# Kernel optimization log

Hardware: AMD Instinct MI355X
Metric: run time of the kernel (lower is better)

Reference implementation:

```python
import jax, jax.numpy as jnp
import numpy as np
from jax import lax

NUM_CLASSES = 5
NUM_TASKS = 20
CONV_CHANS = [(64, 3), (64, 64), (128, 64), (128, 128), (256, 128), (256, 256)]  # (out, in)


def setup_inputs() -> dict:
    key = jax.random.key(0)
    ks = jax.random.split(key, 16)
    B = 512
    x = jax.random.normal(ks[0], (B, 3, 32, 32), dtype=jnp.float32)
    tid = jax.random.randint(ks[1], (B,), 0, NUM_TASKS)
    inp = {"x": x, "tid": tid}
    for i, (oc, ic) in enumerate(CONV_CHANS):
        fan_in = ic * 9
        inp[f"w{i}"] = jax.random.normal(ks[2 + 2 * i], (oc, ic, 3, 3), dtype=jnp.float32) * np.float32((2.0 / fan_in) ** 0.5)
        inp[f"b{i}"] = jnp.zeros((oc,), dtype=jnp.float32)
    inp["cw"] = jax.random.normal(ks[14], (NUM_CLASSES * NUM_TASKS, 4096), dtype=jnp.float32) * np.float32(4096 ** -0.5)
    inp["cb"] = jnp.zeros((NUM_CLASSES * NUM_TASKS,), dtype=jnp.float32)
    return inp


def _conv_relu(x, w, b):
    y = lax.conv_general_dilated(x, w, window_strides=(1, 1), padding='SAME',
                                 dimension_numbers=('NCHW', 'OIHW', 'NCHW'))
    return jax.nn.relu(y + b[None, :, None, None])


def _maxpool2(x):
    return lax.reduce_window(x, -jnp.inf, lax.max, (1, 1, 2, 2), (1, 1, 2, 2), 'VALID')


def _forward(x, tid, ws, bs, cw, cb):
    # VGG cfg [64,64,'M',128,128,'M',256,256,'M']
    h = _conv_relu(x, ws[0], bs[0])
    h = _conv_relu(h, ws[1], bs[1])
    h = _maxpool2(h)
    h = _conv_relu(h, ws[2], bs[2])
    h = _conv_relu(h, ws[3], bs[3])
    h = _maxpool2(h)
    h = _conv_relu(h, ws[4], bs[4])
    h = _conv_relu(h, ws[5], bs[5])
    h = _maxpool2(h)                      # [B, 256, 4, 4]
    feat = h.reshape(h.shape[0], -1)      # [B, 4096], matches torch NCHW flatten
    # Batched task-indexed classifier: gather each sample's 5-row weight block.
    w_sel = cw.reshape(NUM_TASKS, NUM_CLASSES, 4096)[tid]   # [B, 5, 4096]
    b_sel = cb.reshape(NUM_TASKS, NUM_CLASSES)[tid]         # [B, 5]
    return jnp.einsum('bcd,bd->bc', w_sel, feat) + b_sel


def reference(x, tid, w0, b0, w1, b1, w2, b2, w3, b3, w4, b4, w5, b5, cw, cb):
    ws = (w0, w1, w2, w3, w4, w5)
    bs = (b0, b1, b2, b3, b4, b5)
    return _forward(x, tid, ws, bs, cw, cb)
```

## Files before the change

### kernel.cpp

```cpp
#include <hip/hip_runtime.h>


typedef __attribute__((ext_vector_type(8))) short short8;
typedef __attribute__((ext_vector_type(4))) float floatx4;
typedef unsigned int uint;
typedef unsigned short ushort;

__device__ __forceinline__ ushort f2bf(float f) {
    uint u = __float_as_uint(f);
    return (ushort)((u + 0x7fffu + ((u >> 16) & 1u)) >> 16);
}
__device__ __forceinline__ float bf2f(ushort h) {
    return __uint_as_float(((uint)h) << 16);
}

__global__ __launch_bounds__(256) void wtransform_lin(
    const float* __restrict__ src, short* __restrict__ dst, int OC, int IC)
{
    int n = 9 * OC * IC;
    int o = blockIdx.x * 256 + threadIdx.x;
    if (o >= n) return;
    int j    = o & 7;
    int lane = (o >> 3) & 63;
    int r    = o >> 9;
    int G16  = OC >> 4;
    int g    = r % G16;  r /= G16;
    int kk   = r % 9;
    int icb  = r / 9;
    int oc = g * 16 + (lane & 15);
    int ic = icb * 32 + (lane >> 4) * 8 + j;
    dst[o] = (short)f2bf(src[((long)oc * IC + ic) * 9 + kk]);
}

__global__ __launch_bounds__(256) void wtransform0(
    const float* __restrict__ src, short* __restrict__ dst)
{
    int idx = blockIdx.x * 256 + threadIdx.x;
    if (idx >= 64 * 32) return;
    int oc = idx >> 5, k = idx & 31;
    dst[idx] = (k < 27) ? (short)f2bf(src[oc * 27 + k]) : (short)0;
}

__global__ __launch_bounds__(256, 2) void conv0_mfma(
    const float* __restrict__ x, const short* __restrict__ wT0,
    const float* __restrict__ b0, ushort* __restrict__ out)
{
    __shared__ float  s_x[3 * 18 * 34];
    __shared__ ushort s_b[4 * 512 * 8];

    const int tid  = threadIdx.x;
    const int wv   = tid >> 6;
    const int lane = tid & 63;
    const int quad = lane >> 4;
    const int l16  = lane & 15;
    const int b    = blockIdx.x >> 1;
    const int r0   = (blockIdx.x & 1) * 16;

    for (int idx = tid; idx < 3 * 18 * 34; idx += 256) {
        int c   = idx / 612;
        int rem = idx - c * 612;
        int ry  = rem / 34, rx = rem - ry * 34;
        int gy  = r0 + ry - 1, gx = rx - 1;
        float v = 0.f;
        if (gy >= 0 && gy < 32 && gx >= 0 && gx < 32)
            v = x[(((long)b * 3 + c) * 32 + gy) * 32 + gx];
        s_x[idx] = v;
    }
    __syncthreads();

#pragma unroll
    for (int rep = 0; rep < 2; ++rep) {
        int pxl = rep * 256 + tid;
        int py = pxl >> 5, px = pxl & 31;
        ushort v[32];
#pragma unroll
        for (int c = 0; c < 3; ++c)
#pragma unroll
            for (int ky = 0; ky < 3; ++ky)
#pragma unroll
                for (int kx = 0; kx < 3; ++kx)
                    v[c * 9 + ky * 3 + kx] = f2bf(s_x[c * 612 + (py + ky) * 34 + (px + kx)]);
#pragma unroll
        for (int k = 27; k < 32; ++k) v[k] = 0;
#pragma unroll
        for (int q = 0; q < 4; ++q)
            *(uint4*)(&s_b[(q * 512 + pxl) * 8]) = *(const uint4*)(v + q * 8);
    }
    __syncthreads();

    floatx4 acc[4][8];
#pragma unroll
    for (int i = 0; i < 4; ++i)
#pragma unroll
        for (int t = 0; t < 8; ++t) acc[i][t] = (floatx4)0.f;

    short8 afr[4];
#pragma unroll
    for (int i = 0; i < 4; ++i)
        afr[i] = *(const short8*)(wT0 + (i * 16 + l16) * 32 + quad * 8);
#pragma unroll
    for (int t = 0; t < 8; ++t) {
        int pxl = wv * 128 + t * 16 + l16;
        short8 bfr = *(const short8*)(&s_b[(quad * 512 + pxl) * 8]);
#pragma unroll
        for (int i = 0; i < 4; ++i)
            acc[i][t] = __builtin_amdgcn_mfma_f32_16x16x32_bf16(afr[i], bfr, acc[i][t], 0, 0, 0);
    }

#pragma unroll
    for (int i = 0; i < 4; ++i) {
        int oc0 = i * 16 + quad * 4;
        float4 bv = *(const float4*)(b0 + oc0);
#pragma unroll
        for (int t = 0; t < 8; ++t) {
            int pxl = wv * 128 + t * 16 + l16;
            int py = pxl >> 5, px = pxl & 31;
            long dst = ((((long)b * 8 + (oc0 >> 3)) * 32 + r0 + py) * 32 + px) * 8 + (oc0 & 7);
            float v0 = acc[i][t][0] + bv.x;
            float v1 = acc[i][t][1] + bv.y;
            float v2 = acc[i][t][2] + bv.z;
            float v3 = acc[i][t][3] + bv.w;
            ushort o[4];
            o[0] = f2bf(v0 > 0.f ? v0 : 0.f);
            o[1] = f2bf(v1 > 0.f ? v1 : 0.f);
            o[2] = f2bf(v2 > 0.f ? v2 : 0.f);
            o[3] = f2bf(v3 > 0.f ? v3 : 0.f);
            *(uint2*)(out + dst) = *(uint2*)o;
        }
    }
}

template<int IC, int OC, int H, int W, int ROWS, int OCGROUPS, bool POOL>
__global__ __launch_bounds__(256, 2) void conv_so(
    const ushort* __restrict__ act_in,
    const short*  __restrict__ wTs,
    const float*  __restrict__ bias,
    ushort* __restrict__ act_out)
{
    constexpr int WPAD  = W + 2;
    constexpr int RPAD  = ROWS + 2;
    constexpr int UNITS = RPAD * WPAD;
    constexpr int SEGS  = H / ROWS;
    constexpr int C8I   = IC / 8;
    constexpr int CPUP  = C8I + 1;
    constexpr int G16   = OC / 16;
    constexpr int NICB  = IC / 32;
    constexpr int C8O   = OC / 8;
    constexpr int TMAX  = NICB * 9;

    __shared__ ushort s_act[UNITS * CPUP * 8];

    const int tid  = threadIdx.x;
    const int wv   = tid >> 6;
    const int lane = tid & 63;
    const int quad = lane >> 4;
    const int l16  = lane & 15;

    const int b   = blockIdx.x / SEGS;
    const int seg = blockIdx.x - b * SEGS;
    const int r0  = seg * ROWS;
    const int ocg = wv % OCGROUPS;
    const int pxg = wv / OCGROUPS;

    for (int c = tid; c < UNITS * C8I; c += 256) {
        int sub  = c / UNITS;
        int unit = c - sub * UNITS;
        int ry   = unit / WPAD, cx = unit - ry * WPAD;
        int gy   = r0 + ry - 1, gx = cx - 1;
        uint4 val = make_uint4(0, 0, 0, 0);
        if ((unsigned)gy < (unsigned)H && (unsigned)gx < (unsigned)W) {
            long src = ((((long)b * C8I + sub) * H + gy) * W + gx) * 8;
            val = *(const uint4*)(act_in + src);
        }
        *(uint4*)(&s_act[((size_t)unit * CPUP + sub) * 8]) = val;
    }
    __syncthreads();

    floatx4 acc[4][4];
#pragma unroll
    for (int i = 0; i < 4; ++i)
#pragma unroll
        for (int t = 0; t < 4; ++t) acc[i][t] = (floatx4)0.f;

    int bbase[4];
#pragma unroll
    for (int t = 0; t < 4; ++t) {
        int pxl = pxg * 64 + t * 16 + l16;
        int py  = pxl / W, px = pxl - py * W;
        bbase[t] = (py * WPAD + px) * CPUP * 8;
    }

    const short8* wb = (const short8*)wTs;
    short8 afr[4];
#pragma unroll
    for (int i = 0; i < 4; ++i)
        afr[i] = wb[((long)0 * G16 + ocg * 4 + i) * 64 + lane];

    int tl = 0;
    for (int icb = 0; icb < NICB; ++icb) {
#pragma unroll
        for (int kk = 0; kk < 9; ++kk) {
            const int ky = kk / 3, kx = kk - ky * 3;
            const int koff = ((ky * WPAD + kx) * CPUP + icb * 4 + quad) * 8;
            short8 bfr[4];
#pragma unroll
            for (int t = 0; t < 4; ++t)
                bfr[t] = *(const short8*)(&s_act[bbase[t] + koff]);
            int tn = (tl + 1 < TMAX) ? tl + 1 : tl;
            short8 afrN[4];
#pragma unroll
            for (int i = 0; i < 4; ++i)
                afrN[i] = wb[((long)tn * G16 + ocg * 4 + i) * 64 + lane];
#pragma unroll
            for (int i = 0; i < 4; ++i)
#pragma unroll
                for (int t = 0; t < 4; ++t)
                    acc[i][t] = __builtin_amdgcn_mfma_f32_16x16x32_bf16(
                        afr[i], bfr[t], acc[i][t], 0, 0, 0);
#pragma unroll
            for (int i = 0; i < 4; ++i) afr[i] = afrN[i];
            ++tl;
        }
    }

    if constexpr (!POOL) {
#pragma unroll
        for (int i = 0; i < 4; ++i) {
            int oc0 = ocg * 64 + i * 16 + quad * 4;
            float4 bv = *(const float4*)(bias + oc0);
#pragma unroll
            for (int t = 0; t < 4; ++t) {
                int pxl = pxg * 64 + t * 16 + l16;
                int py  = pxl / W, px = pxl - py * W;
                long dst = ((((long)b * C8O + (oc0 >> 3)) * H + r0 + py) * W + px) * 8 + (oc0 & 7);
                float v0 = acc[i][t][0] + bv.x;
                float v1 = acc[i][t][1] + bv.y;
                float v2 = acc[i][t][2] + bv.z;
                float v3 = acc[i][t][3] + bv.w;
                ushort o[4];
                o[0] = f2bf(v0 > 0.f ? v0 : 0.f);
                o[1] = f2bf(v1 > 0.f ? v1 : 0.f);
                o[2] = f2bf(v2 > 0.f ? v2 : 0.f);
                o[3] = f2bf(v3 > 0.f ? v3 : 0.f);
                *(uint2*)(act_out + dst) = *(uint2*)o;
            }
        }
    } else {
        __syncthreads();
        ushort* s_pool = s_act;
        constexpr int PSTR = OC + 8;
        static_assert(ROWS * W * PSTR <= UNITS * CPUP * 8, "pool scratch fits");
#pragma unroll
        for (int i = 0; i < 4; ++i) {
            int oc0 = ocg * 64 + i * 16 + quad * 4;
            float4 bv = *(const float4*)(bias + oc0);
#pragma unroll
            for (int t = 0; t < 4; ++t) {
                int pxl = pxg * 64 + t * 16 + l16;
                float v0 = acc[i][t][0] + bv.x;
                float v1 = acc[i][t][1] + bv.y;
                float v2 = acc[i][t][2] + bv.z;
                float v3 = acc[i][t][3] + bv.w;
                ushort o[4];
                o[0] = f2bf(v0 > 0.f ? v0 : 0.f);
                o[1] = f2bf(v1 > 0.f ? v1 : 0.f);
                o[2] = f2bf(v2 > 0.f ? v2 : 0.f);
                o[3] = f2bf(v3 > 0.f ? v3 : 0.f);
                *(uint2*)(&s_pool[pxl * PSTR + oc0]) = *(uint2*)o;
            }
        }
        __syncthreads();
        constexpr int PH = ROWS / 2, PW = W / 2, HOT = H / 2;
        const int pr0 = r0 / 2;
        for (int u = tid; u < PH * PW * C8O; u += 256) {
            int c8 = u % C8O;
            int pp = u / C8O;
            int xo = pp % PW, yo = pp / PW;
            const ushort* p00 = &s_pool[((2 * yo) * W + 2 * xo) * PSTR + c8 * 8];
            uint4 q0 = *(const uint4*)(p00);
            uint4 q1 = *(const uint4*)(p00 + PSTR);
            uint4 q2 = *(const uint4*)(p00 + W * PSTR);
            uint4 q3 = *(const uint4*)(p00 + W * PSTR + PSTR);
            const ushort* a0 = (const ushort*)&q0;
            const ushort* a1 = (const ushort*)&q1;
            const ushort* a2 = (const ushort*)&q2;
            const ushort* a3 = (const ushort*)&q3;
            ushort r[8];
#pragma unroll
            for (int j = 0; j < 8; ++j) {
                ushort m0 = a0[j] > a1[j] ? a0[j] : a1[j];
                ushort m1 = a2[j] > a3[j] ? a2[j] : a3[j];
                r[j] = m0 > m1 ? m0 : m1;
            }
            long dst = ((((long)b * C8O + c8) * HOT + pr0 + yo) * PW + xo) * 8;
            *(uint4*)(act_out + dst) = *(uint4*)r;
        }
    }
}

__global__ __launch_bounds__(256) void classifier_k(
    const ushort* __restrict__ feat, const int* __restrict__ tids,
    const float* __restrict__ cw, const float* __restrict__ cb,
    float* __restrict__ out, int B)
{
    int g = blockIdx.x * 256 + threadIdx.x;
    int wid = g >> 6, lane = g & 63;
    if (wid >= B * 5) return;
    int b = wid / 5, c = wid - b * 5;
    int t = tids[b];
    const float* wrow = cw + (long)(t * 5 + c) * 4096;
    const ushort* f = feat + (long)b * 4096;
    float s = 0.f;
#pragma unroll 4
    for (int d = lane; d < 4096; d += 64) {
        int fidx = (((d >> 7) * 16) + (d & 15)) * 8 + ((d >> 4) & 7);
        s += wrow[d] * bf2f(f[fidx]);
    }
#pragma unroll
    for (int off = 32; off > 0; off >>= 1) s += __shfl_down(s, off, 64);
    if (lane == 0) out[wid] = s + cb[t * 5 + c];
}

extern "C" void kernel_launch(void* const* d_in, const int* in_sizes, int n_in,
                              void* d_out, int out_size, void* d_ws, size_t ws_size,
                              hipStream_t stream)
{
    const float* x   = (const float*)d_in[0];
    const int*   tid = (const int*)d_in[1];
    const float* w0 = (const float*)d_in[2];  const float* b0 = (const float*)d_in[3];
    const float* w1 = (const float*)d_in[4];  const float* b1 = (const float*)d_in[5];
    const float* w2 = (const float*)d_in[6];  const float* b2 = (const float*)d_in[7];
    const float* w3 = (const float*)d_in[8];  const float* b3 = (const float*)d_in[9];
    const float* w4 = (const float*)d_in[10]; const float* b4 = (const float*)d_in[11];
    const float* w5 = (const float*)d_in[12]; const float* b5 = (const float*)d_in[13];
    const float* cw = (const float*)d_in[14];
    const float* cb = (const float*)d_in[15];
    float* outp = (float*)d_out;

    const int B = in_sizes[0] / (3 * 32 * 32);

    short* wt0  = (short*)d_ws;
    short* wts1 = wt0 + 2048;
    short* wts2 = wts1 + 36864;
    short* wts3 = wts2 + 73728;
    short* wts4 = wts3 + 147456;
    short* wts5 = wts4 + 294912;
    const size_t WT_HW = 2048 + 36864 + 73728 + 147456 + 294912 + 589824;
    const size_t fixed_bytes = WT_HW * 2;

    int Bc = B;
    while (Bc > 2 && fixed_bytes + (size_t)Bc * 2 * 65536 * 2 > ws_size) Bc >>= 1;
    if (Bc < 2) Bc = 2;

    ushort* bufA = (ushort*)((short*)d_ws + WT_HW);
    ushort* bufB = bufA + (size_t)Bc * 65536;

    wtransform0<<<(64 * 32 + 255) / 256, 256, 0, stream>>>(w0, wt0);
    wtransform_lin<<<(9 * 64 * 64 + 255) / 256, 256, 0, stream>>>(w1, wts1, 64, 64);
    wtransform_lin<<<(9 * 128 * 64 + 255) / 256, 256, 0, stream>>>(w2, wts2, 128, 64);
    wtransform_lin<<<(9 * 128 * 128 + 255) / 256, 256, 0, stream>>>(w3, wts3, 128, 128);
    wtransform_lin<<<(9 * 256 * 128 + 255) / 256, 256, 0, stream>>>(w4, wts4, 256, 128);
    wtransform_lin<<<(9 * 256 * 256 + 255) / 256, 256, 0, stream>>>(w5, wts5, 256, 256);

    for (int cb0 = 0; cb0 < B; cb0 += Bc) {
        const float* xc = x + (size_t)cb0 * 3 * 32 * 32;
        const int* tidc = tid + cb0;
        float* outc = outp + (size_t)cb0 * 5;

        conv0_mfma<<<Bc * 2, 256, 0, stream>>>(xc, wt0, b0, bufA);
        conv_so<64, 64, 32, 32, 8, 1, true><<<Bc * 4, 256, 0, stream>>>(bufA, wts1, b1, bufB);
        conv_so<64, 128, 16, 16, 8, 2, false><<<Bc * 2, 256, 0, stream>>>(bufB, wts2, b2, bufA);
        conv_so<128, 128, 16, 16, 8, 2, true><<<Bc * 2, 256, 0, stream>>>(bufA, wts3, b3, bufB);
        conv_so<128, 256, 8, 8, 8, 4, false><<<Bc, 256, 0, stream>>>(bufB, wts4, b4, bufA);
        conv_so<256, 256, 8, 8, 8, 4, true><<<Bc, 256, 0, stream>>>(bufA, wts5, b5, bufB);
        classifier_k<<<(Bc * 5 * 64 + 255) / 256, 256, 0, stream>>>(bufB, tidc, cw, cb, outc, Bc);
    }
}
```

Baseline: 316.0 us.

## Deepen weight prefetch to three stages, raise occupancy, fuse weight transforms

The conv kernel now keeps a three-deep ring of weight fragments in registers, issuing each global load three kernel taps ahead instead of one, to hide global-load latency behind the MFMAs. Launch bounds are raised to three blocks per SM, which caps registers per thread even though the deeper prefetch needs more of them, so spilling is a risk. The six weight-transform launches are merged into one kernel to cut launch overhead. The ring index uses kk%3 inside the unrolled 9-tap loop, so it is compile-time and the ring stays in registers.

```diff
diff --git a/kernel.cpp b/kernel.cpp
--- a/kernel.cpp
+++ b/kernel.cpp
@@ -14,12 +14,9 @@
     return __uint_as_float(((uint)h) << 16);
 }
 
-__global__ __launch_bounds__(256) void wtransform_lin(
-    const float* __restrict__ src, short* __restrict__ dst, int OC, int IC)
-{
-    int n = 9 * OC * IC;
-    int o = blockIdx.x * 256 + threadIdx.x;
-    if (o >= n) return;
+__device__ __forceinline__ void wlin_one(
+    const float* __restrict__ src, short* __restrict__ dst, int OC, int IC, int o)
+{
     int j    = o & 7;
     int lane = (o >> 3) & 63;
     int r    = o >> 9;
@@ -32,13 +29,37 @@
     dst[o] = (short)f2bf(src[((long)oc * IC + ic) * 9 + kk]);
 }
 
-__global__ __launch_bounds__(256) void wtransform0(
-    const float* __restrict__ src, short* __restrict__ dst)
+#define N_W0 2048
+#define N_W1 36864
+#define N_W2 73728
+#define N_W3 147456
+#define N_W4 294912
+#define N_W5 589824
+#define N_WT_TOTAL (N_W0 + N_W1 + N_W2 + N_W3 + N_W4 + N_W5)
+
+__global__ __launch_bounds__(256) void wtransform_all(
+    const float* __restrict__ w0, const float* __restrict__ w1,
+    const float* __restrict__ w2, const float* __restrict__ w3,
+    const float* __restrict__ w4, const float* __restrict__ w5,
+    short* __restrict__ wt0, short* __restrict__ wts1, short* __restrict__ wts2,
+    short* __restrict__ wts3, short* __restrict__ wts4, short* __restrict__ wts5)
 {
     int idx = blockIdx.x * 256 + threadIdx.x;
-    if (idx >= 64 * 32) return;
-    int oc = idx >> 5, k = idx & 31;
-    dst[idx] = (k < 27) ? (short)f2bf(src[oc * 27 + k]) : (short)0;
+    if (idx < N_W0) {
+        int oc = idx >> 5, k = idx & 31;
+        wt0[idx] = (k < 27) ? (short)f2bf(w0[oc * 27 + k]) : (short)0;
+        return;
+    }
+    idx -= N_W0;
+    if (idx < N_W1) { wlin_one(w1, wts1, 64, 64, idx); return; }
+    idx -= N_W1;
+    if (idx < N_W2) { wlin_one(w2, wts2, 128, 64, idx); return; }
+    idx -= N_W2;
+    if (idx < N_W3) { wlin_one(w3, wts3, 128, 128, idx); return; }
+    idx -= N_W3;
+    if (idx < N_W4) { wlin_one(w4, wts4, 256, 128, idx); return; }
+    idx -= N_W4;
+    wlin_one(w5, wts5, 256, 256, idx);
 }
 
 __global__ __launch_bounds__(256, 2) void conv0_mfma(
@@ -131,7 +152,7 @@
 }
 
 template<int IC, int OC, int H, int W, int ROWS, int OCGROUPS, bool POOL>
-__global__ __launch_bounds__(256, 2) void conv_so(
+__global__ __launch_bounds__(256, 3) void conv_so(
     const ushort* __restrict__ act_in,
     const short*  __restrict__ wTs,
     const float*  __restrict__ bias,
@@ -191,34 +212,38 @@
     }
 
     const short8* wb = (const short8*)wTs;
-    short8 afr[4];
-#pragma unroll
-    for (int i = 0; i < 4; ++i)
-        afr[i] = wb[((long)0 * G16 + ocg * 4 + i) * 64 + lane];
+    const int  wbase = (ocg * 4) * 64 + lane;
+    const long WSTEP = (long)G16 * 64;
+
+    short8 wpipe[3][4];
+#pragma unroll
+    for (int d = 0; d < 3; ++d)
+#pragma unroll
+        for (int i = 0; i < 4; ++i)
+            wpipe[d][i] = wb[(long)d * WSTEP + wbase + i * 64];
 
     int tl = 0;
     for (int icb = 0; icb < NICB; ++icb) {
 #pragma unroll
         for (int kk = 0; kk < 9; ++kk) {
             const int ky = kk / 3, kx = kk - ky * 3;
-            const int koff = ((ky * WPAD + kx) * CPUP + icb * 4 + quad) * 8;
+            const int koff = ((ky * WPAD + kx) * CPUP + quad) * 8 + icb * 32;
             short8 bfr[4];
 #pragma unroll
             for (int t = 0; t < 4; ++t)
                 bfr[t] = *(const short8*)(&s_act[bbase[t] + koff]);
-            int tn = (tl + 1 < TMAX) ? tl + 1 : tl;
-            short8 afrN[4];
-#pragma unroll
-            for (int i = 0; i < 4; ++i)
-                afrN[i] = wb[((long)tn * G16 + ocg * 4 + i) * 64 + lane];
+            const int slot = kk % 3;
 #pragma unroll
             for (int i = 0; i < 4; ++i)
 #pragma unroll
                 for (int t = 0; t < 4; ++t)
                     acc[i][t] = __builtin_amdgcn_mfma_f32_16x16x32_bf16(
-                        afr[i], bfr[t], acc[i][t], 0, 0, 0);
-#pragma unroll
-            for (int i = 0; i < 4; ++i) afr[i] = afrN[i];
+                        wpipe[slot][i], bfr[t], acc[i][t], 0, 0, 0);
+            int tn = tl + 3;
+            if (tn >= TMAX) tn = 0;
+#pragma unroll
+            for (int i = 0; i < 4; ++i)
+                wpipe[slot][i] = wb[(long)tn * WSTEP + wbase + i * 64];
             ++tl;
         }
     }
@@ -340,12 +365,12 @@
     const int B = in_sizes[0] / (3 * 32 * 32);
 
     short* wt0  = (short*)d_ws;
-    short* wts1 = wt0 + 2048;
-    short* wts2 = wts1 + 36864;
-    short* wts3 = wts2 + 73728;
-    short* wts4 = wts3 + 147456;
-    short* wts5 = wts4 + 294912;
-    const size_t WT_HW = 2048 + 36864 + 73728 + 147456 + 294912 + 589824;
+    short* wts1 = wt0 + N_W0;
+    short* wts2 = wts1 + N_W1;
+    short* wts3 = wts2 + N_W2;
+    short* wts4 = wts3 + N_W3;
+    short* wts5 = wts4 + N_W4;
+    const size_t WT_HW = N_WT_TOTAL;
     const size_t fixed_bytes = WT_HW * 2;
 
     int Bc = B;
@@ -355,12 +380,8 @@
     ushort* bufA = (ushort*)((short*)d_ws + WT_HW);
     ushort* bufB = bufA + (size_t)Bc * 65536;
 
-    wtransform0<<<(64 * 32 + 255) / 256, 256, 0, stream>>>(w0, wt0);
-    wtransform_lin<<<(9 * 64 * 64 + 255) / 256, 256, 0, stream>>>(w1, wts1, 64, 64);
-    wtransform_lin<<<(9 * 128 * 64 + 255) / 256, 256, 0, stream>>>(w2, wts2, 128, 64);
-    wtransform_lin<<<(9 * 128 * 128 + 255) / 256, 256, 0, stream>>>(w3, wts3, 128, 128);
-    wtransform_lin<<<(9 * 256 * 128 + 255) / 256, 256, 0, stream>>>(w4, wts4, 256, 128);
-    wtransform_lin<<<(9 * 256 * 256 + 255) / 256, 256, 0, stream>>>(w5, wts5, 256, 256);
+    wtransform_all<<<(N_WT_TOTAL + 255) / 256, 256, 0, stream>>>(
+        w0, w1, w2, w3, w4, w5, wt0, wts1, wts2, wts3, wts4, wts5);
 
     for (int cb0 = 0; cb0 < B; cb0 += Bc) {
         const float* xc = x + (size_t)cb0 * 3 * 32 * 32;
```

Measured after the change: 285.6 us. 9.6% less time.
